# Kernel tuning notes

Measured on AMD Instinct MI355X. Metric: run time of the kernel, lower is better.

## Reference

```python
import jax, jax.numpy as jnp
import numpy as np

N, D_IN, D_OUT = 8192, 128, 128

def setup_inputs() -> dict:
    key = jax.random.key(0)
    k1, k2, k3 = jax.random.split(key, 3)
    x = jax.random.normal(k1, (N, D_IN), dtype=jnp.float32)
    adjacency_matrix = jax.random.uniform(k2, (N, N), dtype=jnp.float32)
    weight = jax.random.normal(k3, (D_IN, D_OUT), dtype=jnp.float32) * (1.0 / np.sqrt(D_IN))
    return {"x": x, "adjacency_matrix": adjacency_matrix, "weight": weight}

def reference(x, adjacency_matrix, weight):
    # degree = row sums of A; D^{-1} A  ==  row-normalized adjacency.
    # (torch.inverse of the diagonal degree matrix is just 1/degree.)
    degree = jnp.sum(adjacency_matrix, axis=-1, keepdims=True)  # [N, 1]
    # Fuse: out = D^{-1} (A @ x) @ W  -- avoids materializing normalized A? 
    # Faithful math: (D^{-1} A) x W == D^{-1} (A x) W since D^{-1} is diagonal.
    ax = adjacency_matrix @ x                                   # [N, D_IN]
    out = (ax / degree) @ weight                                # [N, D_OUT]
    return out
```

## Files before the change

### kernel.cpp

```cpp
#include <hip/hip_runtime.h>
#include <hip/hip_bf16.h>

#define NN 8192
#define DD 128

typedef __attribute__((ext_vector_type(4))) float f32x4;
typedef __attribute__((ext_vector_type(8))) short bf16x8;

__device__ __forceinline__ short f2bf(float f) {
  __hip_bfloat16 h = __float2bfloat16(f);
  return __builtin_bit_cast(short, h);
}

__device__ __forceinline__ void async_copy16(void* lds, const void* g) {
  __builtin_amdgcn_global_load_lds(
      (const __attribute__((address_space(1))) void*)g,
      (__attribute__((address_space(3))) void*)lds, 16, 0, 0);
}

__global__ __launch_bounds__(256) void xw_kernel(
    const float* __restrict__ x, const float* __restrict__ W,
    short* __restrict__ yT)
{
  __shared__ float xs[32][129];
  const int t  = threadIdx.x;
  const int k0 = blockIdx.x * 32;

  #pragma unroll
  for (int i = 0; i < 4; ++i) {
    int idx = i * 256 + t;
    int row = idx >> 5;
    int c4  = (idx & 31) * 4;
    f32x4 v = *(const f32x4*)(x + (size_t)(k0 + row) * DD + c4);
    xs[row][c4 + 0] = v[0]; xs[row][c4 + 1] = v[1];
    xs[row][c4 + 2] = v[2]; xs[row][c4 + 3] = v[3];
  }
  __syncthreads();

  const int kl = t & 31;
  const int g  = t >> 5;
  float acc[16];
  #pragma unroll
  for (int j = 0; j < 16; ++j) acc[j] = 0.f;

  for (int d = 0; d < 128; ++d) {
    float xv = xs[kl][d];
    const float* wr = W + d * DD + g * 16;
    f32x4 w0 = *(const f32x4*)(wr);
    f32x4 w1 = *(const f32x4*)(wr + 4);
    f32x4 w2 = *(const f32x4*)(wr + 8);
    f32x4 w3 = *(const f32x4*)(wr + 12);
    #pragma unroll
    for (int j = 0; j < 4; ++j) {
      acc[j]      += xv * w0[j];
      acc[4 + j]  += xv * w1[j];
      acc[8 + j]  += xv * w2[j];
      acc[12 + j] += xv * w3[j];
    }
  }
  #pragma unroll
  for (int j = 0; j < 16; ++j) {
    int n = g * 16 + j;
    yT[(size_t)n * NN + k0 + kl] = f2bf(acc[j]);
  }
}

__global__ __launch_bounds__(512, 4) void gcn_main(
    const float* __restrict__ A, const short* __restrict__ yT,
    float* __restrict__ part, float* __restrict__ degpart)
{
  __shared__ float Abuf[2][128 * 32];
  __shared__ short Ybuf[2][128 * 32];

  const int tid   = threadIdx.x;
  const int l     = tid & 63;
  const int w     = tid >> 6;
  const int ks    = blockIdx.x & 7;
  const int mg    = blockIdx.x >> 3;
  const int R0    = mg * 128;
  const int kbase = ks * 1024;
  const int l15   = l & 15;
  const int kg    = l >> 4;

  const int a_r8  = l >> 3;
  const int a_grp = (l & 7) ^ a_r8;
  const int y_r16 = l >> 2;
  const int y_grp = (l & 3) ^ (y_r16 & 3);

  const float* gA0 = A  + (size_t)(R0 + (w * 2 + 0) * 8 + a_r8) * NN + a_grp * 4;
  const float* gA1 = A  + (size_t)(R0 + (w * 2 + 1) * 8 + a_r8) * NN + a_grp * 4;
  const short* gY  = yT + (size_t)(w * 16 + y_r16) * NN + y_grp * 8;

  const int arow    = w * 16 + l15;
  const int asw     = arow & 7;
  const int aoff_lo = arow * 32 + ((((kg << 1))     ^ asw) << 2);
  const int aoff_hi = arow * 32 + ((((kg << 1) | 1) ^ asw) << 2);
  const int yoff    = l15 * 32 + ((kg ^ (l15 & 3)) << 3);

  f32x4 acc[8];
  #pragma unroll
  for (int n = 0; n < 8; ++n) acc[n] = (f32x4)0.f;
  float deg = 0.f;

  {
    async_copy16(&Abuf[0][(w * 2 + 0) * 256], gA0 + kbase);
    async_copy16(&Abuf[0][(w * 2 + 1) * 256], gA1 + kbase);
    async_copy16(&Ybuf[0][w * 512],           gY  + kbase);
  }
  __syncthreads();

  for (int s = 0; s < 32; ++s) {
    const int cur = s & 1;
    if (s < 31) {
      const int k = kbase + (s + 1) * 32;
      async_copy16(&Abuf[cur ^ 1][(w * 2 + 0) * 256], gA0 + k);
      async_copy16(&Abuf[cur ^ 1][(w * 2 + 1) * 256], gA1 + k);
      async_copy16(&Ybuf[cur ^ 1][w * 512],           gY  + k);
    }

    const float* Ab = Abuf[cur];
    const short* Yb = Ybuf[cur];

    f32x4 alo = *(const f32x4*)&Ab[aoff_lo];
    f32x4 ahi = *(const f32x4*)&Ab[aoff_hi];

    deg += (alo[0] + alo[1]) + (alo[2] + alo[3])
         + (ahi[0] + ahi[1]) + (ahi[2] + ahi[3]);

    bf16x8 a;
    #pragma unroll
    for (int j = 0; j < 4; ++j) {
      a[j]     = f2bf(alo[j]);
      a[4 + j] = f2bf(ahi[j]);
    }

    #pragma unroll
    for (int n = 0; n < 8; ++n) {
      bf16x8 b = *(const bf16x8*)&Yb[n * 512 + yoff];
      acc[n] = __builtin_amdgcn_mfma_f32_16x16x32_bf16(a, b, acc[n], 0, 0, 0);
    }

    __syncthreads();
  }

  deg += __shfl_xor(deg, 16);
  deg += __shfl_xor(deg, 32);
  if (l < 16)
    degpart[(size_t)ks * NN + R0 + w * 16 + l] = deg;

  float* pbase = part + (size_t)ks * NN * DD + (size_t)(R0 + w * 16) * DD;
  #pragma unroll
  for (int n = 0; n < 8; ++n)
    #pragma unroll
    for (int i = 0; i < 4; ++i)
      __builtin_nontemporal_store(acc[n][i],
          pbase + (size_t)(kg * 4 + i) * DD + n * 16 + l15);
}

__global__ __launch_bounds__(256) void reduce_kernel(
    const float* __restrict__ part, const float* __restrict__ degpart,
    float* __restrict__ out)
{
  const int idx = blockIdx.x * 256 + threadIdx.x;
  const int m   = idx >> 5;
  const int c4  = (idx & 31) * 4;

  f32x4 s = (f32x4)0.f;
  float d = 0.f;
  #pragma unroll
  for (int ks = 0; ks < 8; ++ks) {
    f32x4 v = *(const f32x4*)(part + (size_t)ks * NN * DD + (size_t)m * DD + c4);
    s[0] += v[0]; s[1] += v[1]; s[2] += v[2]; s[3] += v[3];
    d += degpart[(size_t)ks * NN + m];
  }
  f32x4 r;
  r[0] = s[0] / d; r[1] = s[1] / d; r[2] = s[2] / d; r[3] = s[3] / d;
  *(f32x4*)(out + (size_t)m * DD + c4) = r;
}

extern "C" void kernel_launch(void* const* d_in, const int* in_sizes, int n_in,
                              void* d_out, int out_size, void* d_ws, size_t ws_size,
                              hipStream_t stream) {
  const float* x = (const float*)d_in[0];
  const float* A = (const float*)d_in[1];
  const float* W = (const float*)d_in[2];
  float* out = (float*)d_out;

  char* ws = (char*)d_ws;
  short* yT      = (short*)ws;
  float* part    = (float*)(ws + (2u << 20));
  float* degpart = (float*)(ws + (2u << 20) + (32u << 20));

  xw_kernel<<<256, 256, 0, stream>>>(x, W, yT);
  gcn_main<<<512, 512, 0, stream>>>(A, yT, part, degpart);
  reduce_kernel<<<1024, 256, 0, stream>>>(part, degpart, out);
}
```

Baseline: 102.5 us.

## Triple-buffer A and Y tiles with explicit vmcnt waits in gcn_main

Replaces the double-buffered LDS pipeline with a three-stage ring, so two tiles are always in flight while one is computed. Each step now waits only for its own loads with s_waitcnt vmcnt(6/3/0) rather than a full drain. The goal is to hide more global-load latency on the streaming read of the adjacency matrix. In exchange it uses 1.5x the LDS, which can limit blocks per CU, and adds a second barrier per step to protect buffer reuse.

```diff
diff --git a/kernel.cpp b/kernel.cpp
--- a/kernel.cpp
+++ b/kernel.cpp
@@ -69,8 +69,8 @@
     const float* __restrict__ A, const short* __restrict__ yT,
     float* __restrict__ part, float* __restrict__ degpart)
 {
-  __shared__ float Abuf[2][128 * 32];
-  __shared__ short Ybuf[2][128 * 32];
+  __shared__ float Abuf[3][128 * 32];
+  __shared__ short Ybuf[3][128 * 32];
 
   const int tid   = threadIdx.x;
   const int l     = tid & 63;
@@ -102,25 +102,14 @@
   for (int n = 0; n < 8; ++n) acc[n] = (f32x4)0.f;
   float deg = 0.f;
 
-  {
-    async_copy16(&Abuf[0][(w * 2 + 0) * 256], gA0 + kbase);
-    async_copy16(&Abuf[0][(w * 2 + 1) * 256], gA1 + kbase);
-    async_copy16(&Ybuf[0][w * 512],           gY  + kbase);
-  }
-  __syncthreads();
-
-  for (int s = 0; s < 32; ++s) {
-    const int cur = s & 1;
-    if (s < 31) {
-      const int k = kbase + (s + 1) * 32;
-      async_copy16(&Abuf[cur ^ 1][(w * 2 + 0) * 256], gA0 + k);
-      async_copy16(&Abuf[cur ^ 1][(w * 2 + 1) * 256], gA1 + k);
-      async_copy16(&Ybuf[cur ^ 1][w * 512],           gY  + k);
-    }
-
-    const float* Ab = Abuf[cur];
-    const short* Yb = Ybuf[cur];
-
+#define STAGE(buf, step) do {                                        \
+    const int _k = kbase + (step) * 32;                              \
+    async_copy16(&Abuf[buf][(w * 2 + 0) * 256], gA0 + _k);           \
+    async_copy16(&Abuf[buf][(w * 2 + 1) * 256], gA1 + _k);           \
+    async_copy16(&Ybuf[buf][w * 512],           gY  + _k);           \
+  } while (0)
+
+  auto compute = [&](const float* Ab, const short* Yb) {
     f32x4 alo = *(const f32x4*)&Ab[aoff_lo];
     f32x4 ahi = *(const f32x4*)&Ab[aoff_hi];
 
@@ -139,9 +128,32 @@
       bf16x8 b = *(const bf16x8*)&Yb[n * 512 + yoff];
       acc[n] = __builtin_amdgcn_mfma_f32_16x16x32_bf16(a, b, acc[n], 0, 0, 0);
     }
-
-    __syncthreads();
-  }
+  };
+
+  STAGE(0, 0);
+  STAGE(1, 1);
+  STAGE(2, 2);
+
+  for (int st = 0; st < 30; st += 3) {
+    #pragma unroll
+    for (int j = 0; j < 3; ++j) {
+      asm volatile("s_waitcnt vmcnt(6)" ::: "memory");
+      __builtin_amdgcn_s_barrier();
+      compute(Abuf[j], Ybuf[j]);
+      __builtin_amdgcn_s_barrier();
+      __builtin_amdgcn_sched_barrier(0);
+      if (st + j < 29)
+        STAGE(j, st + j + 3);
+    }
+  }
+  asm volatile("s_waitcnt vmcnt(3)" ::: "memory");
+  __builtin_amdgcn_s_barrier();
+  compute(Abuf[0], Ybuf[0]);
+  __builtin_amdgcn_s_barrier();
+  asm volatile("s_waitcnt vmcnt(0)" ::: "memory");
+  __builtin_amdgcn_s_barrier();
+  compute(Abuf[1], Ybuf[1]);
+#undef STAGE
 
   deg += __shfl_xor(deg, 16);
   deg += __shfl_xor(deg, 32);
```

New measurement: 101.2 us. No clear change (-1.3%).

## Restructure GCN main loop with deeper A staging and direct global Y loads

Applied to the files above, without the earlier changes.

The main kernel now stages 128-column tiles of A (64 KB per buffer) with async LDS copies. It waits with explicit vmcnt counts instead of __syncthreads and reads the bf16 XW operand straight from global/L2 rather than staging it in LDS. The split-K factor drops from 8 to 4, which halves the grid and shrinks the partial-sum buffer and reduction. The xw kernel also caches W in shared memory. Each block now uses 128 KB of LDS, so occupancy drops and fewer blocks run per CU, and Y global loads can add latency to the MFMA loop.

```diff
diff --git a/kernel.cpp b/kernel.cpp
--- a/kernel.cpp
+++ b/kernel.cpp
@@ -23,9 +23,15 @@
     short* __restrict__ yT)
 {
   __shared__ float xs[32][129];
+  __shared__ float Ws[128 * 128];
   const int t  = threadIdx.x;
   const int k0 = blockIdx.x * 32;
 
+  #pragma unroll
+  for (int i = 0; i < 16; ++i) {
+    int idx = (i * 256 + t) * 4;
+    *(f32x4*)&Ws[idx] = *(const f32x4*)(W + idx);
+  }
   #pragma unroll
   for (int i = 0; i < 4; ++i) {
     int idx = i * 256 + t;
@@ -45,7 +51,7 @@
 
   for (int d = 0; d < 128; ++d) {
     float xv = xs[kl][d];
-    const float* wr = W + d * DD + g * 16;
+    const float* wr = &Ws[d * 128 + g * 16];
     f32x4 w0 = *(const f32x4*)(wr);
     f32x4 w1 = *(const f32x4*)(wr + 4);
     f32x4 w2 = *(const f32x4*)(wr + 8);
@@ -65,83 +71,88 @@
   }
 }
 
-__global__ __launch_bounds__(512, 4) void gcn_main(
+__global__ __launch_bounds__(512, 2) void gcn_main(
     const float* __restrict__ A, const short* __restrict__ yT,
     float* __restrict__ part, float* __restrict__ degpart)
 {
-  __shared__ float Abuf[2][128 * 32];
-  __shared__ short Ybuf[2][128 * 32];
+  __shared__ float Abuf[2][128 * 128];
 
   const int tid   = threadIdx.x;
   const int l     = tid & 63;
   const int w     = tid >> 6;
-  const int ks    = blockIdx.x & 7;
-  const int mg    = blockIdx.x >> 3;
+  const int ks    = blockIdx.x & 3;
+  const int mg    = blockIdx.x >> 2;
   const int R0    = mg * 128;
-  const int kbase = ks * 1024;
+  const int kbase = ks * 2048;
   const int l15   = l & 15;
   const int kg    = l >> 4;
 
-  const int a_r8  = l >> 3;
-  const int a_grp = (l & 7) ^ a_r8;
-  const int y_r16 = l >> 2;
-  const int y_grp = (l & 3) ^ (y_r16 & 3);
-
-  const float* gA0 = A  + (size_t)(R0 + (w * 2 + 0) * 8 + a_r8) * NN + a_grp * 4;
-  const float* gA1 = A  + (size_t)(R0 + (w * 2 + 1) * 8 + a_r8) * NN + a_grp * 4;
-  const short* gY  = yT + (size_t)(w * 16 + y_r16) * NN + y_grp * 8;
-
-  const int arow    = w * 16 + l15;
-  const int asw     = arow & 7;
-  const int aoff_lo = arow * 32 + ((((kg << 1))     ^ asw) << 2);
-  const int aoff_hi = arow * 32 + ((((kg << 1) | 1) ^ asw) << 2);
-  const int yoff    = l15 * 32 + ((kg ^ (l15 & 3)) << 3);
+  const int sh   = l >> 5;
+  const int sgrp = l & 31;
+  const float* gA[8];
+  #pragma unroll
+  for (int j = 0; j < 8; ++j) {
+    const int r = w * 16 + 2 * j + sh;
+    gA[j] = A + (size_t)(R0 + r) * NN + kbase
+              + ((sgrp ^ ((2 * j) & 7) ^ sh) << 2);
+  }
+
+  const int arow   = w * 16 + l15;
+  const int axor   = arow & 7;
+  const int arow_l = arow * 128;
+  const short* yrow = yT + (size_t)l15 * NN + kg * 8;
 
   f32x4 acc[8];
   #pragma unroll
   for (int n = 0; n < 8; ++n) acc[n] = (f32x4)0.f;
   float deg = 0.f;
 
-  {
-    async_copy16(&Abuf[0][(w * 2 + 0) * 256], gA0 + kbase);
-    async_copy16(&Abuf[0][(w * 2 + 1) * 256], gA1 + kbase);
-    async_copy16(&Ybuf[0][w * 512],           gY  + kbase);
-  }
-  __syncthreads();
-
-  for (int s = 0; s < 32; ++s) {
-    const int cur = s & 1;
-    if (s < 31) {
-      const int k = kbase + (s + 1) * 32;
-      async_copy16(&Abuf[cur ^ 1][(w * 2 + 0) * 256], gA0 + k);
-      async_copy16(&Abuf[cur ^ 1][(w * 2 + 1) * 256], gA1 + k);
-      async_copy16(&Ybuf[cur ^ 1][w * 512],           gY  + k);
+#define STAGE(buf, step) do {                                              \
+    _Pragma("unroll")                                                      \
+    for (int j = 0; j < 8; ++j)                                            \
+      async_copy16(&Abuf[buf][(w * 16 + 2 * j) * 128],                     \
+                   gA[j] + (step) * 128);                                  \
+  } while (0)
+
+  STAGE(0, 0);
+  STAGE(1, 1);
+
+  for (int s = 0; s < 16; ++s) {
+    __builtin_amdgcn_sched_barrier(0);
+    if (s < 15) asm volatile("s_waitcnt vmcnt(8)" ::: "memory");
+    else        asm volatile("s_waitcnt vmcnt(0)" ::: "memory");
+    __builtin_amdgcn_sched_barrier(0);
+
+    const float* Ab = &Abuf[s & 1][0];
+    const int koff  = kbase + s * 128;
+    #pragma unroll
+    for (int ss = 0; ss < 4; ++ss) {
+      const int g0 = ss * 8 + kg * 2;
+      f32x4 alo = *(const f32x4*)&Ab[arow_l + (((g0    ) ^ axor) << 2)];
+      f32x4 ahi = *(const f32x4*)&Ab[arow_l + (((g0 + 1) ^ axor) << 2)];
+
+      deg += (alo[0] + alo[1]) + (alo[2] + alo[3])
+           + (ahi[0] + ahi[1]) + (ahi[2] + ahi[3]);
+
+      bf16x8 a;
+      #pragma unroll
+      for (int j = 0; j < 4; ++j) {
+        a[j]     = f2bf(alo[j]);
+        a[4 + j] = f2bf(ahi[j]);
+      }
+
+      #pragma unroll
+      for (int n = 0; n < 8; ++n) {
+        bf16x8 b = *(const bf16x8*)(yrow + (size_t)(n * 16) * NN
+                                         + koff + ss * 32);
+        acc[n] = __builtin_amdgcn_mfma_f32_16x16x32_bf16(a, b, acc[n], 0, 0, 0);
+      }
     }
 
-    const float* Ab = Abuf[cur];
-    const short* Yb = Ybuf[cur];
-
-    f32x4 alo = *(const f32x4*)&Ab[aoff_lo];
-    f32x4 ahi = *(const f32x4*)&Ab[aoff_hi];
-
-    deg += (alo[0] + alo[1]) + (alo[2] + alo[3])
-         + (ahi[0] + ahi[1]) + (ahi[2] + ahi[3]);
-
-    bf16x8 a;
-    #pragma unroll
-    for (int j = 0; j < 4; ++j) {
-      a[j]     = f2bf(alo[j]);
-      a[4 + j] = f2bf(ahi[j]);
-    }
-
-    #pragma unroll
-    for (int n = 0; n < 8; ++n) {
-      bf16x8 b = *(const bf16x8*)&Yb[n * 512 + yoff];
-      acc[n] = __builtin_amdgcn_mfma_f32_16x16x32_bf16(a, b, acc[n], 0, 0, 0);
-    }
-
-    __syncthreads();
-  }
+    __builtin_amdgcn_sched_barrier(0);
+    if (s + 2 < 16) STAGE(s & 1, s + 2);
+  }
+#undef STAGE
 
   deg += __shfl_xor(deg, 16);
   deg += __shfl_xor(deg, 32);
@@ -168,7 +179,7 @@
   f32x4 s = (f32x4)0.f;
   float d = 0.f;
   #pragma unroll
-  for (int ks = 0; ks < 8; ++ks) {
+  for (int ks = 0; ks < 4; ++ks) {
     f32x4 v = *(const f32x4*)(part + (size_t)ks * NN * DD + (size_t)m * DD + c4);
     s[0] += v[0]; s[1] += v[1]; s[2] += v[2]; s[3] += v[3];
     d += degpart[(size_t)ks * NN + m];
@@ -189,9 +200,9 @@
   char* ws = (char*)d_ws;
   short* yT      = (short*)ws;
   float* part    = (float*)(ws + (2u << 20));
-  float* degpart = (float*)(ws + (2u << 20) + (32u << 20));
+  float* degpart = (float*)(ws + (2u << 20) + (16u << 20));
 
   xw_kernel<<<256, 256, 0, stream>>>(x, W, yT);
-  gcn_main<<<512, 512, 0, stream>>>(A, yT, part, degpart);
+  gcn_main<<<256, 512, 0, stream>>>(A, yT, part, degpart);
   reduce_kernel<<<1024, 256, 0, stream>>>(part, degpart, out);
 }
```

Measured after the change: 153.5 us. +49.8%, slower.
